# Kernel tuning notes

Hardware: AMD Instinct MI355X
Metric: run time of the kernel (lower is better)

The kernel has to match this reference:

```python
import jax, jax.numpy as jnp
import numpy as np

D_MODEL = 512
NHEAD = 8
HEAD_DIM = D_MODEL // NHEAD
D_FF = 2048
EPS = 1e-5


def _layernorm(x, w, b):
    mu = jnp.mean(x, axis=-1, keepdims=True)
    var = jnp.mean(jnp.square(x - mu), axis=-1, keepdims=True)
    return (x - mu) * jax.lax.rsqrt(var + EPS) * w + b


def setup_inputs() -> dict:
    key = jax.random.key(0)
    ks = jax.random.split(key, 10)
    B, L = 4, 2048
    x = jax.random.normal(ks[0], (B, L, D_MODEL), dtype=jnp.float32)
    attn_bias = jax.random.normal(ks[1], (1, NHEAD, L, L), dtype=jnp.float32)
    s = 0.02
    # weights stored as (in, out): y = x @ w + b
    wq = jax.random.normal(ks[2], (D_MODEL, D_MODEL), dtype=jnp.float32) * s
    wk = jax.random.normal(ks[3], (D_MODEL, D_MODEL), dtype=jnp.float32) * s
    wv = jax.random.normal(ks[4], (D_MODEL, D_MODEL), dtype=jnp.float32) * s
    wo = jax.random.normal(ks[5], (D_MODEL, D_MODEL), dtype=jnp.float32) * s
    w1 = jax.random.normal(ks[6], (D_MODEL, D_FF), dtype=jnp.float32) * s
    w2 = jax.random.normal(ks[7], (D_FF, D_MODEL), dtype=jnp.float32) * s
    z = lambda n: jnp.zeros((n,), dtype=jnp.float32)
    o = lambda n: jnp.ones((n,), dtype=jnp.float32)
    return {
        "x": x, "attn_bias": attn_bias,
        "ln1_w": o(D_MODEL), "ln1_b": z(D_MODEL),
        "ln2_w": o(D_MODEL), "ln2_b": z(D_MODEL),
        "wq": wq, "bq": z(D_MODEL), "wk": wk, "bk": z(D_MODEL),
        "wv": wv, "bv": z(D_MODEL), "wo": wo, "bo": z(D_MODEL),
        "w1": w1, "b1": z(D_FF), "w2": w2, "b2": z(D_MODEL),
    }


def reference(x, attn_bias, ln1_w, ln1_b, ln2_w, ln2_b,
              wq, bq, wk, bk, wv, bv, wo, bo, w1, b1, w2, b2):
    B, L, D = x.shape
    H, Dh = NHEAD, HEAD_DIM

    # --- self-attention block (pre-LN) ---
    h = _layernorm(x, ln1_w, ln1_b)
    q = (h @ wq + bq).reshape(B, L, H, Dh)
    k = (h @ wk + bk).reshape(B, L, H, Dh)
    v = (h @ wv + bv).reshape(B, L, H, Dh)
    scores = jnp.einsum('bqhd,bkhd->bhqk', q, k) * (Dh ** -0.5)
    scores = scores + attn_bias  # broadcast over batch if bias has leading 1
    attn = jax.nn.softmax(scores, axis=-1)
    o = jnp.einsum('bhqk,bkhd->bqhd', attn, v).reshape(B, L, D)
    x = x + (o @ wo + bo)

    # --- feed-forward block (pre-LN, exact GELU like torch nn.GELU) ---
    h2 = _layernorm(x, ln2_w, ln2_b)
    ff = jax.nn.gelu(h2 @ w1 + b1, approximate=False) @ w2 + b2
    return x + ff
```

## Files before the change

### kernel.cpp

```cpp
#include <hip/hip_runtime.h>
#include <hip/hip_bf16.h>

typedef __bf16 bf16x8 __attribute__((ext_vector_type(8)));
typedef float  f32x4  __attribute__((ext_vector_type(4)));
typedef unsigned short us8 __attribute__((ext_vector_type(8)));

__device__ inline unsigned short f2bf(float f) {
    unsigned u = __builtin_bit_cast(unsigned, f);
    u += 0x7fffu + ((u >> 16) & 1u);
    return (unsigned short)(u >> 16);
}

__device__ inline bf16x8 load_frag(const unsigned short* p) {
    return *reinterpret_cast<const bf16x8*>(p);
}

__device__ inline void gload_lds16(const unsigned short* g, unsigned short* l) {
    __builtin_amdgcn_global_load_lds(
        (const __attribute__((address_space(1))) void*)g,
        (__attribute__((address_space(3))) void*)l, 16, 0, 0);
}

__global__ void prep_kernel(const float* __restrict__ wq, const float* __restrict__ wk,
                            const float* __restrict__ wv, const float* __restrict__ wo,
                            const float* __restrict__ w1, const float* __restrict__ w2,
                            const float* __restrict__ bq, const float* __restrict__ bk,
                            const float* __restrict__ bv,
                            unsigned short* __restrict__ wqkvT, unsigned short* __restrict__ woT,
                            unsigned short* __restrict__ w1T, unsigned short* __restrict__ w2T,
                            float* __restrict__ biasqkv) {
    int bid = blockIdx.x;
    int tx = threadIdx.x, ty = threadIdx.y;
    if (bid >= 3072) {
        int i = (bid - 3072) * 256 + ty * 32 + tx;
        float v = (i < 512) ? bq[i] : ((i < 1024) ? bk[i - 512] : bv[i - 1024]);
        biasqkv[i] = v;
        return;
    }
    const float* src; unsigned short* dst; int K, N, tile;
    if (bid < 256)       { src = wq; dst = wqkvT;          K = 512;  N = 512;  tile = bid; }
    else if (bid < 512)  { src = wk; dst = wqkvT + 262144; K = 512;  N = 512;  tile = bid - 256; }
    else if (bid < 768)  { src = wv; dst = wqkvT + 524288; K = 512;  N = 512;  tile = bid - 512; }
    else if (bid < 1024) { src = wo; dst = woT;            K = 512;  N = 512;  tile = bid - 768; }
    else if (bid < 2048) { src = w1; dst = w1T;            K = 512;  N = 2048; tile = bid - 1024; }
    else                 { src = w2; dst = w2T;            K = 2048; N = 512;  tile = bid - 2048; }
    int ntx = N >> 5;
    int n0 = (tile % ntx) * 32, k0 = (tile / ntx) * 32;
    __shared__ float tilebuf[32][33];
#pragma unroll
    for (int i = 0; i < 4; ++i)
        tilebuf[ty + 8 * i][tx] = src[(size_t)(k0 + ty + 8 * i) * N + n0 + tx];
    __syncthreads();
#pragma unroll
    for (int i = 0; i < 4; ++i)
        dst[(size_t)(n0 + ty + 8 * i) * K + k0 + tx] = f2bf(tilebuf[tx][ty + 8 * i]);
}

__global__ __launch_bounds__(256) void ln_kernel(const float* __restrict__ x,
                                                 const float* __restrict__ w,
                                                 const float* __restrict__ b,
                                                 unsigned short* __restrict__ out) {
    int wave = threadIdx.x >> 6, lane = threadIdx.x & 63;
    size_t row = (size_t)blockIdx.x * 4 + wave;
    const float* xp = x + row * 512 + lane * 8;
    float4 v0 = *reinterpret_cast<const float4*>(xp);
    float4 v1 = *reinterpret_cast<const float4*>(xp + 4);
    float s = (v0.x + v0.y) + (v0.z + v0.w) + (v1.x + v1.y) + (v1.z + v1.w);
    float qq = v0.x * v0.x + v0.y * v0.y + v0.z * v0.z + v0.w * v0.w
             + v1.x * v1.x + v1.y * v1.y + v1.z * v1.z + v1.w * v1.w;
#pragma unroll
    for (int off = 1; off < 64; off <<= 1) {
        s += __shfl_xor(s, off, 64);
        qq += __shfl_xor(qq, off, 64);
    }
    float mu = s * (1.0f / 512.0f);
    float var = qq * (1.0f / 512.0f) - mu * mu;
    float rstd = rsqrtf(var + 1e-5f);
    int c = lane * 8;
    float4 w0 = *reinterpret_cast<const float4*>(w + c);
    float4 w1 = *reinterpret_cast<const float4*>(w + c + 4);
    float4 b0 = *reinterpret_cast<const float4*>(b + c);
    float4 b1 = *reinterpret_cast<const float4*>(b + c + 4);
    us8 r;
    r[0] = f2bf((v0.x - mu) * rstd * w0.x + b0.x);
    r[1] = f2bf((v0.y - mu) * rstd * w0.y + b0.y);
    r[2] = f2bf((v0.z - mu) * rstd * w0.z + b0.z);
    r[3] = f2bf((v0.w - mu) * rstd * w0.w + b0.w);
    r[4] = f2bf((v1.x - mu) * rstd * w1.x + b1.x);
    r[5] = f2bf((v1.y - mu) * rstd * w1.y + b1.y);
    r[6] = f2bf((v1.z - mu) * rstd * w1.z + b1.z);
    r[7] = f2bf((v1.w - mu) * rstd * w1.w + b1.w);
    *reinterpret_cast<us8*>(out + row * 512 + c) = r;
}

template <int EPI>
__global__ __launch_bounds__(256) void gemm128(const unsigned short* __restrict__ A,
                                               const unsigned short* __restrict__ BT,
                                               const float* __restrict__ bias, void* Cout,
                                               const float* __restrict__ res, int M, int N, int K) {
    __shared__ unsigned short As[128 * 32];
    __shared__ unsigned short Bs[128 * 32];
    int tid = threadIdx.x;
    int lane = tid & 63, wave = tid >> 6;
    int quad = lane >> 4, l16 = lane & 15;
    int wm = (wave >> 1) * 64, wn = (wave & 1) * 64;
    int m0 = blockIdx.y * 128, n0 = blockIdx.x * 128;

    int c0 = tid, c1 = tid + 256;
    const unsigned short* ag0 = A + (size_t)(m0 + (c0 >> 2)) * K + (c0 & 3) * 8;
    const unsigned short* ag1 = A + (size_t)(m0 + (c1 >> 2)) * K + (c1 & 3) * 8;
    const unsigned short* bg0 = BT + (size_t)(n0 + (c0 >> 2)) * K + (c0 & 3) * 8;
    const unsigned short* bg1 = BT + (size_t)(n0 + (c1 >> 2)) * K + (c1 & 3) * 8;
    unsigned short* al0 = As + c0 * 8;
    unsigned short* al1 = As + c1 * 8;
    unsigned short* bl0 = Bs + c0 * 8;
    unsigned short* bl1 = Bs + c1 * 8;

    f32x4 acc[4][4] = {};
    for (int k0 = 0; k0 < K; k0 += 32) {
        __syncthreads();
        gload_lds16(ag0 + k0, al0);
        gload_lds16(ag1 + k0, al1);
        gload_lds16(bg0 + k0, bl0);
        gload_lds16(bg1 + k0, bl1);
        __syncthreads();
        bf16x8 af[4], bf[4];
#pragma unroll
        for (int i = 0; i < 4; ++i)
            af[i] = load_frag(As + (wm + i * 16 + l16) * 32 + quad * 8);
#pragma unroll
        for (int j = 0; j < 4; ++j)
            bf[j] = load_frag(Bs + (wn + j * 16 + l16) * 32 + quad * 8);
#pragma unroll
        for (int i = 0; i < 4; ++i)
#pragma unroll
            for (int j = 0; j < 4; ++j)
                acc[i][j] = __builtin_amdgcn_mfma_f32_16x16x32_bf16(af[i], bf[j], acc[i][j], 0, 0, 0);
    }

#pragma unroll
    for (int i = 0; i < 4; ++i) {
#pragma unroll
        for (int j = 0; j < 4; ++j) {
#pragma unroll
            for (int r = 0; r < 4; ++r) {
                int m = m0 + wm + i * 16 + quad * 4 + r;
                int n = n0 + wn + j * 16 + l16;
                float val = acc[i][j][r] + bias[n];
                size_t idx = (size_t)m * N + n;
                if (EPI == 0) {
                    ((unsigned short*)Cout)[idx] = f2bf(val);
                } else if (EPI == 1) {
                    ((float*)Cout)[idx] = val + res[idx];
                } else {
                    float g = 0.5f * val * (1.0f + erff(val * 0.70710678118654752f));
                    ((unsigned short*)Cout)[idx] = f2bf(g);
                }
            }
        }
    }
}

__global__ __launch_bounds__(256) void gemm128_ff2(const unsigned short* __restrict__ A,
                                                   const unsigned short* __restrict__ BT,
                                                   const float* __restrict__ bias,
                                                   float* __restrict__ C, int M, int N, int K) {
    __shared__ unsigned short As[128 * 32];
    __shared__ unsigned short Bs[128 * 32];
    int tid = threadIdx.x;
    int lane = tid & 63, wave = tid >> 6;
    int quad = lane >> 4, l16 = lane & 15;
    int wm = (wave >> 1) * 64, wn = (wave & 1) * 64;
    int m0 = blockIdx.y * 128, n0 = blockIdx.x * 128;
    int kbeg = blockIdx.z * (K >> 1), kend = kbeg + (K >> 1);

    int c0 = tid, c1 = tid + 256;
    const unsigned short* ag0 = A + (size_t)(m0 + (c0 >> 2)) * K + (c0 & 3) * 8;
    const unsigned short* ag1 = A + (size_t)(m0 + (c1 >> 2)) * K + (c1 & 3) * 8;
    const unsigned short* bg0 = BT + (size_t)(n0 + (c0 >> 2)) * K + (c0 & 3) * 8;
    const unsigned short* bg1 = BT + (size_t)(n0 + (c1 >> 2)) * K + (c1 & 3) * 8;
    unsigned short* al0 = As + c0 * 8;
    unsigned short* al1 = As + c1 * 8;
    unsigned short* bl0 = Bs + c0 * 8;
    unsigned short* bl1 = Bs + c1 * 8;

    f32x4 acc[4][4] = {};
    for (int k0 = kbeg; k0 < kend; k0 += 32) {
        __syncthreads();
        gload_lds16(ag0 + k0, al0);
        gload_lds16(ag1 + k0, al1);
        gload_lds16(bg0 + k0, bl0);
        gload_lds16(bg1 + k0, bl1);
        __syncthreads();
        bf16x8 af[4], bf[4];
#pragma unroll
        for (int i = 0; i < 4; ++i)
            af[i] = load_frag(As + (wm + i * 16 + l16) * 32 + quad * 8);
#pragma unroll
        for (int j = 0; j < 4; ++j)
            bf[j] = load_frag(Bs + (wn + j * 16 + l16) * 32 + quad * 8);
#pragma unroll
        for (int i = 0; i < 4; ++i)
#pragma unroll
            for (int j = 0; j < 4; ++j)
                acc[i][j] = __builtin_amdgcn_mfma_f32_16x16x32_bf16(af[i], bf[j], acc[i][j], 0, 0, 0);
    }

#pragma unroll
    for (int i = 0; i < 4; ++i) {
#pragma unroll
        for (int j = 0; j < 4; ++j) {
#pragma unroll
            for (int r = 0; r < 4; ++r) {
                int m = m0 + wm + i * 16 + quad * 4 + r;
                int n = n0 + wn + j * 16 + l16;
                float val = acc[i][j][r] + (blockIdx.z == 0 ? bias[n] : 0.0f);
                atomicAdd(&C[(size_t)m * N + n], val);
            }
        }
    }
}

__global__ __launch_bounds__(256) void attn_kernel(const unsigned short* __restrict__ qkv,
                                                   const float* __restrict__ bias,
                                                   unsigned short* __restrict__ o) {
    __shared__ unsigned short Ks[64 * 64];
    __shared__ unsigned short VTs[64 * 72];
    __shared__ unsigned short Ps[4 * 16 * 64];
    const int tid = threadIdx.x;
    const int lane = tid & 63, wave = tid >> 6, quad = lane >> 4, l16 = lane & 15;
    const int qb = blockIdx.x, h = blockIdx.y, b = blockIdx.z;
    const int qw = qb * 64 + wave * 16;

    const unsigned short* qbase = qkv + ((size_t)(b * 2048 + qw + l16)) * 1536 + h * 64 + quad * 8;
    bf16x8 qf0 = load_frag(qbase);
    bf16x8 qf1 = load_frag(qbase + 32);

    f32x4 Oacc[4] = {};
    float lsum[4] = {};

    const int krow0 = wave * 16 + (lane >> 3);
    const int kc_phys = lane & 7;
    unsigned short* kl = Ks + krow0 * 64 + kc_phys * 8;
    const int ksw = (kc_phys ^ (krow0 & 7)) << 3;

    const int srow = tid >> 2, q4 = tid & 3, sd0 = q4 * 16;
    const int vt_c = (srow >> 3) ^ (q4 << 1);
    unsigned short* vtw = VTs + sd0 * 72 + vt_c * 8 + (srow & 7);

    const float* brow = bias + (size_t)h * 2048 * 2048 + (size_t)(qw + quad * 4) * 2048 + l16;

    const float S2 = 0.18033688011112042f;
    const float K2 = 1.4426950408889634f;
    const float C2 = -11.541560327111707f;

    uint4 vt0, vt1;
    float bbf[4][4];
    {
        const unsigned short* kg = qkv + ((size_t)(b * 2048 + krow0)) * 1536 + 512 + h * 64 + ksw;
        gload_lds16(kg, kl);
        gload_lds16(kg + (size_t)8 * 1536, kl + 8 * 64);
        const unsigned short* vg = qkv + ((size_t)(b * 2048 + srow)) * 1536 + 1024 + h * 64 + sd0;
        vt0 = *reinterpret_cast<const uint4*>(vg);
        vt1 = *reinterpret_cast<const uint4*>(vg + 8);
#pragma unroll
        for (int t = 0; t < 4; ++t)
#pragma unroll
            for (int r = 0; r < 4; ++r)
                bbf[t][r] = fmaf(brow[(size_t)r * 2048 + t * 16], K2, C2);
    }

    for (int kt = 0; kt < 32; ++kt) {
        __syncthreads();
        {
            unsigned short vtmp[16];
            *reinterpret_cast<uint4*>(vtmp) = vt0;
            *reinterpret_cast<uint4*>(vtmp + 8) = vt1;
#pragma unroll
            for (int j = 0; j < 16; ++j) vtw[j * 72] = vtmp[j];
        }
        __syncthreads();

#pragma unroll
        for (int t = 0; t < 4; ++t) {
            f32x4 c = {};
            bf16x8 b0 = load_frag(Ks + (t * 16 + l16) * 64 + ((quad ^ (l16 & 7)) << 3));
            bf16x8 b1 = load_frag(Ks + (t * 16 + l16) * 64 + (((quad + 4) ^ (l16 & 7)) << 3));
            c = __builtin_amdgcn_mfma_f32_16x16x32_bf16(qf0, b0, c, 0, 0, 0);
            c = __builtin_amdgcn_mfma_f32_16x16x32_bf16(qf1, b1, c, 0, 0, 0);
            int pc = (t * 2 + (l16 >> 3)) ^ (quad * 2);
            unsigned short* pw = Ps + wave * 1024 + quad * 256 + pc * 8 + (l16 & 7);
#pragma unroll
            for (int r = 0; r < 4; ++r) {
                float e = __builtin_amdgcn_exp2f(fmaf(c[r], S2, bbf[t][r]));
                lsum[r] += e;
                pw[r * 64] = f2bf(e);
            }
        }
        __syncthreads();

        {
            int kb2 = (kt < 31 ? kt + 1 : 31) * 64;
            const unsigned short* kg = qkv + ((size_t)(b * 2048 + kb2 + krow0)) * 1536 + 512 + h * 64 + ksw;
            gload_lds16(kg, kl);
            gload_lds16(kg + (size_t)8 * 1536, kl + 8 * 64);
            const unsigned short* vg = qkv + ((size_t)(b * 2048 + kb2 + srow)) * 1536 + 1024 + h * 64 + sd0;
            vt0 = *reinterpret_cast<const uint4*>(vg);
            vt1 = *reinterpret_cast<const uint4*>(vg + 8);
#pragma unroll
            for (int t = 0; t < 4; ++t)
#pragma unroll
                for (int r = 0; r < 4; ++r)
                    bbf[t][r] = fmaf(brow[(size_t)r * 2048 + kb2 + t * 16], K2, C2);
        }

        bf16x8 pa0 = load_frag(Ps + wave * 1024 + l16 * 64 + ((quad ^ ((l16 >> 2) << 1)) << 3));
        bf16x8 pa1 = load_frag(Ps + wave * 1024 + l16 * 64 + (((quad + 4) ^ ((l16 >> 2) << 1)) << 3));
#pragma unroll
        for (int t = 0; t < 4; ++t) {
            bf16x8 vb0 = load_frag(VTs + (t * 16 + l16) * 72 + ((quad ^ (t * 2)) << 3));
            bf16x8 vb1 = load_frag(VTs + (t * 16 + l16) * 72 + (((quad + 4) ^ (t * 2)) << 3));
            Oacc[t] = __builtin_amdgcn_mfma_f32_16x16x32_bf16(pa0, vb0, Oacc[t], 0, 0, 0);
            Oacc[t] = __builtin_amdgcn_mfma_f32_16x16x32_bf16(pa1, vb1, Oacc[t], 0, 0, 0);
        }
    }

#pragma unroll
    for (int off = 1; off < 16; off <<= 1)
#pragma unroll
        for (int r = 0; r < 4; ++r) lsum[r] += __shfl_xor(lsum[r], off, 64);
#pragma unroll
    for (int r = 0; r < 4; ++r) {
        float inv = 1.0f / lsum[r];
        int qg = qw + quad * 4 + r;
        unsigned short* op = o + ((size_t)(b * 2048 + qg)) * 512 + h * 64;
#pragma unroll
        for (int t = 0; t < 4; ++t) op[t * 16 + l16] = f2bf(Oacc[t][r] * inv);
    }
}

extern "C" void kernel_launch(void* const* d_in, const int* in_sizes, int n_in,
                              void* d_out, int out_size, void* d_ws, size_t ws_size,
                              hipStream_t stream) {
    const float* x      = (const float*)d_in[0];
    const float* abias  = (const float*)d_in[1];
    const float* ln1_w  = (const float*)d_in[2];
    const float* ln1_b  = (const float*)d_in[3];
    const float* ln2_w  = (const float*)d_in[4];
    const float* ln2_b  = (const float*)d_in[5];
    const float* wq     = (const float*)d_in[6];
    const float* bq     = (const float*)d_in[7];
    const float* wk     = (const float*)d_in[8];
    const float* bk     = (const float*)d_in[9];
    const float* wv     = (const float*)d_in[10];
    const float* bv     = (const float*)d_in[11];
    const float* wo     = (const float*)d_in[12];
    const float* bo     = (const float*)d_in[13];
    const float* w1     = (const float*)d_in[14];
    const float* b1     = (const float*)d_in[15];
    const float* w2     = (const float*)d_in[16];
    const float* b2     = (const float*)d_in[17];
    float* out = (float*)d_out;

    char* ws = (char*)d_ws;
    unsigned short* wqkvT  = (unsigned short*)(ws + 0);
    unsigned short* woT    = (unsigned short*)(ws + 1572864);
    unsigned short* w1T    = (unsigned short*)(ws + 2097152);
    unsigned short* w2T    = (unsigned short*)(ws + 4194304);
    float*          biasqkv= (float*)(ws + 6291456);
    unsigned short* hbuf   = (unsigned short*)(ws + 6297600);
    unsigned short* qkv    = (unsigned short*)(ws + 14686208);
    unsigned short* o_attn = (unsigned short*)(ws + 39852032);
    unsigned short* ff1    = (unsigned short*)(ws + 48240640);

    prep_kernel<<<3078, dim3(32, 8), 0, stream>>>(wq, wk, wv, wo, w1, w2, bq, bk, bv,
                                                  wqkvT, woT, w1T, w2T, biasqkv);
    ln_kernel<<<2048, 256, 0, stream>>>(x, ln1_w, ln1_b, hbuf);
    gemm128<0><<<dim3(12, 64), 256, 0, stream>>>(hbuf, wqkvT, biasqkv, qkv, nullptr, 8192, 1536, 512);
    attn_kernel<<<dim3(32, 8, 4), 256, 0, stream>>>(qkv, abias, o_attn);
    gemm128<1><<<dim3(4, 64), 256, 0, stream>>>(o_attn, woT, bo, out, x, 8192, 512, 512);
    ln_kernel<<<2048, 256, 0, stream>>>(out, ln2_w, ln2_b, hbuf);
    gemm128<2><<<dim3(16, 64), 256, 0, stream>>>(hbuf, w1T, b1, ff1, nullptr, 8192, 2048, 512);
    gemm128_ff2<<<dim3(4, 64, 2), 256, 0, stream>>>(ff1, w2T, b2, out, 8192, 512, 2048);
}
```

Baseline: 494.9 us.

## Rework GEMMs with 64-wide swizzled K tiles, V-transposed layout, double-buffered attention

The GEMM core now stages 64-wide K tiles with an XOR-swizzled LDS layout. Each GEMM gets its own specialised epilogue kernel, and occupancy hints are added through launch bounds. The QKV projection writes V pre-transposed to a separate buffer, so attention can load K and V^T straight into double-buffered LDS with async loads instead of transposing V through registers each tile. The output projection becomes a split-K atomic GEMM that adds into an output first seeded with x by a device copy. This adds an extra memcpy and atomics in exchange for fewer barriers and less LDS traffic.

```diff
diff --git a/kernel.cpp b/kernel.cpp
--- a/kernel.cpp
+++ b/kernel.cpp
@@ -93,233 +93,237 @@
     *reinterpret_cast<us8*>(out + row * 512 + c) = r;
 }
 
-template <int EPI>
-__global__ __launch_bounds__(256) void gemm128(const unsigned short* __restrict__ A,
-                                               const unsigned short* __restrict__ BT,
-                                               const float* __restrict__ bias, void* Cout,
-                                               const float* __restrict__ res, int M, int N, int K) {
-    __shared__ unsigned short As[128 * 32];
-    __shared__ unsigned short Bs[128 * 32];
-    int tid = threadIdx.x;
-    int lane = tid & 63, wave = tid >> 6;
-    int quad = lane >> 4, l16 = lane & 15;
-    int wm = (wave >> 1) * 64, wn = (wave & 1) * 64;
-    int m0 = blockIdx.y * 128, n0 = blockIdx.x * 128;
-
-    int c0 = tid, c1 = tid + 256;
-    const unsigned short* ag0 = A + (size_t)(m0 + (c0 >> 2)) * K + (c0 & 3) * 8;
-    const unsigned short* ag1 = A + (size_t)(m0 + (c1 >> 2)) * K + (c1 & 3) * 8;
-    const unsigned short* bg0 = BT + (size_t)(n0 + (c0 >> 2)) * K + (c0 & 3) * 8;
-    const unsigned short* bg1 = BT + (size_t)(n0 + (c1 >> 2)) * K + (c1 & 3) * 8;
-    unsigned short* al0 = As + c0 * 8;
-    unsigned short* al1 = As + c1 * 8;
-    unsigned short* bl0 = Bs + c0 * 8;
-    unsigned short* bl1 = Bs + c1 * 8;
-
+__device__ __forceinline__ void gemm_core(const unsigned short* __restrict__ A,
+                                          const unsigned short* __restrict__ BT,
+                                          int K, int kbeg, int ksteps,
+                                          int m0, int n0, f32x4 (&acc)[4][4]) {
+    __shared__ unsigned short As[8192];
+    __shared__ unsigned short Bs[8192];
+    const int tid = threadIdx.x;
+    const int lane = tid & 63, wave = tid >> 6;
+    const int quad = lane >> 4, l16 = lane & 15;
+    const int wm = (wave >> 1) * 64, wn = (wave & 1) * 64;
+    const int row0 = tid >> 3;
+    const int jl = (tid & 7) ^ (row0 & 7);
+    const unsigned short* ag = A + (size_t)(m0 + row0) * K + kbeg + jl * 8;
+    const unsigned short* bg = BT + (size_t)(n0 + row0) * K + kbeg + jl * 8;
+    unsigned short* al = As + tid * 8;
+    unsigned short* bl = Bs + tid * 8;
+    const int sw = l16 & 7;
+
+    for (int ks = 0; ks < ksteps; ++ks) {
+        __syncthreads();
+#pragma unroll
+        for (int s = 0; s < 4; ++s) {
+            gload_lds16(ag + (size_t)32 * s * K, al + 2048 * s);
+            gload_lds16(bg + (size_t)32 * s * K, bl + 2048 * s);
+        }
+        ag += 64; bg += 64;
+        __syncthreads();
+#pragma unroll
+        for (int h = 0; h < 2; ++h) {
+            bf16x8 af[4], bf[4];
+#pragma unroll
+            for (int i = 0; i < 4; ++i)
+                af[i] = load_frag(As + (wm + i * 16 + l16) * 64 + (((h * 4 + quad) ^ sw) * 8));
+#pragma unroll
+            for (int j = 0; j < 4; ++j)
+                bf[j] = load_frag(Bs + (wn + j * 16 + l16) * 64 + (((h * 4 + quad) ^ sw) * 8));
+#pragma unroll
+            for (int i = 0; i < 4; ++i)
+#pragma unroll
+                for (int j = 0; j < 4; ++j)
+                    acc[i][j] = __builtin_amdgcn_mfma_f32_16x16x32_bf16(af[i], bf[j], acc[i][j], 0, 0, 0);
+        }
+    }
+}
+
+__global__ __launch_bounds__(256, 3) void gemm_qkv_k(const unsigned short* __restrict__ A,
+                                                     const unsigned short* __restrict__ BT,
+                                                     const float* __restrict__ bias,
+                                                     unsigned short* __restrict__ qk,
+                                                     unsigned short* __restrict__ vT) {
     f32x4 acc[4][4] = {};
-    for (int k0 = 0; k0 < K; k0 += 32) {
-        __syncthreads();
-        gload_lds16(ag0 + k0, al0);
-        gload_lds16(ag1 + k0, al1);
-        gload_lds16(bg0 + k0, bl0);
-        gload_lds16(bg1 + k0, bl1);
-        __syncthreads();
-        bf16x8 af[4], bf[4];
+    const int m0 = blockIdx.y * 128, n0 = blockIdx.x * 128;
+    gemm_core(A, BT, 512, 0, 8, m0, n0, acc);
+    const int tid = threadIdx.x, lane = tid & 63, wave = tid >> 6;
+    const int quad = lane >> 4, l16 = lane & 15;
+    const int wm = (wave >> 1) * 64, wn = (wave & 1) * 64;
+    if (n0 < 1024) {
 #pragma unroll
         for (int i = 0; i < 4; ++i)
-            af[i] = load_frag(As + (wm + i * 16 + l16) * 32 + quad * 8);
-#pragma unroll
-        for (int j = 0; j < 4; ++j)
-            bf[j] = load_frag(Bs + (wn + j * 16 + l16) * 32 + quad * 8);
-#pragma unroll
-        for (int i = 0; i < 4; ++i)
-#pragma unroll
-            for (int j = 0; j < 4; ++j)
-                acc[i][j] = __builtin_amdgcn_mfma_f32_16x16x32_bf16(af[i], bf[j], acc[i][j], 0, 0, 0);
-    }
-
-#pragma unroll
-    for (int i = 0; i < 4; ++i) {
+#pragma unroll
+            for (int j = 0; j < 4; ++j) {
+                int n = n0 + wn + j * 16 + l16;
+                float bn = bias[n];
+#pragma unroll
+                for (int r = 0; r < 4; ++r) {
+                    int m = m0 + wm + i * 16 + quad * 4 + r;
+                    qk[(size_t)m * 1024 + n] = f2bf(acc[i][j][r] + bn);
+                }
+            }
+    } else {
+#pragma unroll
+        for (int i = 0; i < 4; ++i) {
+            int mb = m0 + wm + i * 16 + quad * 4;
+            int bb = mb >> 11, tok = mb & 2047;
+#pragma unroll
+            for (int j = 0; j < 4; ++j) {
+                int n = n0 + wn + j * 16 + l16;
+                float bn = bias[n];
+                int hd = n - 1024;
+                ushort4 pk;
+                pk.x = f2bf(acc[i][j][0] + bn);
+                pk.y = f2bf(acc[i][j][1] + bn);
+                pk.z = f2bf(acc[i][j][2] + bn);
+                pk.w = f2bf(acc[i][j][3] + bn);
+                *reinterpret_cast<ushort4*>(vT + (size_t)(bb * 512 + hd) * 2048 + tok) = pk;
+            }
+        }
+    }
+}
+
+__global__ __launch_bounds__(256, 3) void gemm_gelu_k(const unsigned short* __restrict__ A,
+                                                      const unsigned short* __restrict__ BT,
+                                                      const float* __restrict__ bias,
+                                                      unsigned short* __restrict__ C) {
+    f32x4 acc[4][4] = {};
+    const int m0 = blockIdx.y * 128, n0 = blockIdx.x * 128;
+    gemm_core(A, BT, 512, 0, 8, m0, n0, acc);
+    const int tid = threadIdx.x, lane = tid & 63, wave = tid >> 6;
+    const int quad = lane >> 4, l16 = lane & 15;
+    const int wm = (wave >> 1) * 64, wn = (wave & 1) * 64;
+#pragma unroll
+    for (int i = 0; i < 4; ++i)
 #pragma unroll
         for (int j = 0; j < 4; ++j) {
+            int n = n0 + wn + j * 16 + l16;
+            float bn = bias[n];
 #pragma unroll
             for (int r = 0; r < 4; ++r) {
                 int m = m0 + wm + i * 16 + quad * 4 + r;
-                int n = n0 + wn + j * 16 + l16;
-                float val = acc[i][j][r] + bias[n];
-                size_t idx = (size_t)m * N + n;
-                if (EPI == 0) {
-                    ((unsigned short*)Cout)[idx] = f2bf(val);
-                } else if (EPI == 1) {
-                    ((float*)Cout)[idx] = val + res[idx];
-                } else {
-                    float g = 0.5f * val * (1.0f + erff(val * 0.70710678118654752f));
-                    ((unsigned short*)Cout)[idx] = f2bf(g);
-                }
-            }
-        }
-    }
-}
-
-__global__ __launch_bounds__(256) void gemm128_ff2(const unsigned short* __restrict__ A,
-                                                   const unsigned short* __restrict__ BT,
-                                                   const float* __restrict__ bias,
-                                                   float* __restrict__ C, int M, int N, int K) {
-    __shared__ unsigned short As[128 * 32];
-    __shared__ unsigned short Bs[128 * 32];
-    int tid = threadIdx.x;
-    int lane = tid & 63, wave = tid >> 6;
-    int quad = lane >> 4, l16 = lane & 15;
-    int wm = (wave >> 1) * 64, wn = (wave & 1) * 64;
-    int m0 = blockIdx.y * 128, n0 = blockIdx.x * 128;
-    int kbeg = blockIdx.z * (K >> 1), kend = kbeg + (K >> 1);
-
-    int c0 = tid, c1 = tid + 256;
-    const unsigned short* ag0 = A + (size_t)(m0 + (c0 >> 2)) * K + (c0 & 3) * 8;
-    const unsigned short* ag1 = A + (size_t)(m0 + (c1 >> 2)) * K + (c1 & 3) * 8;
-    const unsigned short* bg0 = BT + (size_t)(n0 + (c0 >> 2)) * K + (c0 & 3) * 8;
-    const unsigned short* bg1 = BT + (size_t)(n0 + (c1 >> 2)) * K + (c1 & 3) * 8;
-    unsigned short* al0 = As + c0 * 8;
-    unsigned short* al1 = As + c1 * 8;
-    unsigned short* bl0 = Bs + c0 * 8;
-    unsigned short* bl1 = Bs + c1 * 8;
-
+                float val = acc[i][j][r] + bn;
+                float g = 0.5f * val * (1.0f + erff(val * 0.70710678118654752f));
+                C[(size_t)m * 2048 + n] = f2bf(g);
+            }
+        }
+}
+
+__global__ __launch_bounds__(256, 3) void gemm_atomic_k(const unsigned short* __restrict__ A,
+                                                        const unsigned short* __restrict__ BT,
+                                                        const float* __restrict__ bias,
+                                                        float* __restrict__ C,
+                                                        int N, int K, int ksteps) {
     f32x4 acc[4][4] = {};
-    for (int k0 = kbeg; k0 < kend; k0 += 32) {
-        __syncthreads();
-        gload_lds16(ag0 + k0, al0);
-        gload_lds16(ag1 + k0, al1);
-        gload_lds16(bg0 + k0, bl0);
-        gload_lds16(bg1 + k0, bl1);
-        __syncthreads();
-        bf16x8 af[4], bf[4];
-#pragma unroll
-        for (int i = 0; i < 4; ++i)
-            af[i] = load_frag(As + (wm + i * 16 + l16) * 32 + quad * 8);
-#pragma unroll
-        for (int j = 0; j < 4; ++j)
-            bf[j] = load_frag(Bs + (wn + j * 16 + l16) * 32 + quad * 8);
-#pragma unroll
-        for (int i = 0; i < 4; ++i)
-#pragma unroll
-            for (int j = 0; j < 4; ++j)
-                acc[i][j] = __builtin_amdgcn_mfma_f32_16x16x32_bf16(af[i], bf[j], acc[i][j], 0, 0, 0);
-    }
-
-#pragma unroll
-    for (int i = 0; i < 4; ++i) {
+    const int m0 = blockIdx.y * 128, n0 = blockIdx.x * 128;
+    const int kbeg = blockIdx.z * ksteps * 64;
+    gemm_core(A, BT, K, kbeg, ksteps, m0, n0, acc);
+    const int tid = threadIdx.x, lane = tid & 63, wave = tid >> 6;
+    const int quad = lane >> 4, l16 = lane & 15;
+    const int wm = (wave >> 1) * 64, wn = (wave & 1) * 64;
+    const bool addb = (blockIdx.z == 0);
+#pragma unroll
+    for (int i = 0; i < 4; ++i)
 #pragma unroll
         for (int j = 0; j < 4; ++j) {
+            int n = n0 + wn + j * 16 + l16;
+            float bn = addb ? bias[n] : 0.0f;
 #pragma unroll
             for (int r = 0; r < 4; ++r) {
                 int m = m0 + wm + i * 16 + quad * 4 + r;
-                int n = n0 + wn + j * 16 + l16;
-                float val = acc[i][j][r] + (blockIdx.z == 0 ? bias[n] : 0.0f);
-                atomicAdd(&C[(size_t)m * N + n], val);
-            }
-        }
-    }
-}
-
-__global__ __launch_bounds__(256) void attn_kernel(const unsigned short* __restrict__ qkv,
-                                                   const float* __restrict__ bias,
-                                                   unsigned short* __restrict__ o) {
-    __shared__ unsigned short Ks[64 * 64];
-    __shared__ unsigned short VTs[64 * 72];
-    __shared__ unsigned short Ps[4 * 16 * 64];
+                atomicAdd(&C[(size_t)m * N + n], acc[i][j][r] + bn);
+            }
+        }
+}
+
+__global__ __launch_bounds__(256, 4) void attn_kernel(const unsigned short* __restrict__ qk,
+                                                      const unsigned short* __restrict__ vT,
+                                                      const float* __restrict__ bias,
+                                                      unsigned short* __restrict__ o) {
+    __shared__ unsigned short Ks[2][4096];
+    __shared__ unsigned short VTs[2][4096];
+    __shared__ unsigned short Ps[4096];
     const int tid = threadIdx.x;
     const int lane = tid & 63, wave = tid >> 6, quad = lane >> 4, l16 = lane & 15;
     const int qb = blockIdx.x, h = blockIdx.y, b = blockIdx.z;
     const int qw = qb * 64 + wave * 16;
 
-    const unsigned short* qbase = qkv + ((size_t)(b * 2048 + qw + l16)) * 1536 + h * 64 + quad * 8;
+    const unsigned short* qbase = qk + (size_t)(b * 2048 + qw + l16) * 1024 + h * 64 + quad * 8;
     bf16x8 qf0 = load_frag(qbase);
     bf16x8 qf1 = load_frag(qbase + 32);
 
     f32x4 Oacc[4] = {};
     float lsum[4] = {};
 
-    const int krow0 = wave * 16 + (lane >> 3);
-    const int kc_phys = lane & 7;
-    unsigned short* kl = Ks + krow0 * 64 + kc_phys * 8;
-    const int ksw = (kc_phys ^ (krow0 & 7)) << 3;
-
-    const int srow = tid >> 2, q4 = tid & 3, sd0 = q4 * 16;
-    const int vt_c = (srow >> 3) ^ (q4 << 1);
-    unsigned short* vtw = VTs + sd0 * 72 + vt_c * 8 + (srow & 7);
+    const int p8 = lane & 7;
+    const int r0 = wave * 16 + (lane >> 3);
+    const int swz = (p8 ^ (r0 & 7)) * 8;
+    const unsigned short* kg = qk + (size_t)(b * 2048 + r0) * 1024 + 512 + h * 64 + swz;
+    const unsigned short* vg = vT + (size_t)(b * 512 + h * 64 + r0) * 2048 + swz;
+    const int ldst = r0 * 64 + p8 * 8;
 
     const float* brow = bias + (size_t)h * 2048 * 2048 + (size_t)(qw + quad * 4) * 2048 + l16;
-
     const float S2 = 0.18033688011112042f;
     const float K2 = 1.4426950408889634f;
     const float C2 = -11.541560327111707f;
 
-    uint4 vt0, vt1;
+    gload_lds16(kg, Ks[0] + ldst);
+    gload_lds16(kg + 8 * 1024, Ks[0] + 512 + ldst);
+    gload_lds16(vg, VTs[0] + ldst);
+    gload_lds16(vg + 8 * 2048, VTs[0] + 512 + ldst);
     float bbf[4][4];
-    {
-        const unsigned short* kg = qkv + ((size_t)(b * 2048 + krow0)) * 1536 + 512 + h * 64 + ksw;
-        gload_lds16(kg, kl);
-        gload_lds16(kg + (size_t)8 * 1536, kl + 8 * 64);
-        const unsigned short* vg = qkv + ((size_t)(b * 2048 + srow)) * 1536 + 1024 + h * 64 + sd0;
-        vt0 = *reinterpret_cast<const uint4*>(vg);
-        vt1 = *reinterpret_cast<const uint4*>(vg + 8);
-#pragma unroll
-        for (int t = 0; t < 4; ++t)
-#pragma unroll
-            for (int r = 0; r < 4; ++r)
-                bbf[t][r] = fmaf(brow[(size_t)r * 2048 + t * 16], K2, C2);
-    }
-
+#pragma unroll
+    for (int t = 0; t < 4; ++t)
+#pragma unroll
+        for (int r = 0; r < 4; ++r)
+            bbf[t][r] = fmaf(brow[(size_t)r * 2048 + t * 16], K2, C2);
+
+    const int sw7 = l16 & 7;
     for (int kt = 0; kt < 32; ++kt) {
+        const int buf = kt & 1;
         __syncthreads();
-        {
-            unsigned short vtmp[16];
-            *reinterpret_cast<uint4*>(vtmp) = vt0;
-            *reinterpret_cast<uint4*>(vtmp + 8) = vt1;
-#pragma unroll
-            for (int j = 0; j < 16; ++j) vtw[j * 72] = vtmp[j];
-        }
-        __syncthreads();
-
+        if (kt < 31) {
+            const unsigned short* kg2 = kg + (size_t)(kt + 1) * 64 * 1024;
+            const unsigned short* vg2 = vg + (kt + 1) * 64;
+            gload_lds16(kg2, Ks[buf ^ 1] + ldst);
+            gload_lds16(kg2 + 8 * 1024, Ks[buf ^ 1] + 512 + ldst);
+            gload_lds16(vg2, VTs[buf ^ 1] + ldst);
+            gload_lds16(vg2 + 8 * 2048, VTs[buf ^ 1] + 512 + ldst);
+        }
 #pragma unroll
         for (int t = 0; t < 4; ++t) {
+            const unsigned short* krow = Ks[buf] + (t * 16 + l16) * 64;
+            bf16x8 kb0 = load_frag(krow + ((quad ^ sw7) * 8));
+            bf16x8 kb1 = load_frag(krow + (((quad + 4) ^ sw7) * 8));
             f32x4 c = {};
-            bf16x8 b0 = load_frag(Ks + (t * 16 + l16) * 64 + ((quad ^ (l16 & 7)) << 3));
-            bf16x8 b1 = load_frag(Ks + (t * 16 + l16) * 64 + (((quad + 4) ^ (l16 & 7)) << 3));
-            c = __builtin_amdgcn_mfma_f32_16x16x32_bf16(qf0, b0, c, 0, 0, 0);
-            c = __builtin_amdgcn_mfma_f32_16x16x32_bf16(qf1, b1, c, 0, 0, 0);
-            int pc = (t * 2 + (l16 >> 3)) ^ (quad * 2);
-            unsigned short* pw = Ps + wave * 1024 + quad * 256 + pc * 8 + (l16 & 7);
+            c = __builtin_amdgcn_mfma_f32_16x16x32_bf16(qf0, kb0, c, 0, 0, 0);
+            c = __builtin_amdgcn_mfma_f32_16x16x32_bf16(qf1, kb1, c, 0, 0, 0);
 #pragma unroll
             for (int r = 0; r < 4; ++r) {
                 float e = __builtin_amdgcn_exp2f(fmaf(c[r], S2, bbf[t][r]));
                 lsum[r] += e;
-                pw[r * 64] = f2bf(e);
+                int m = quad * 4 + r;
+                int phys = (t * 2 + (l16 >> 3)) ^ ((m >> 1) & 7);
+                Ps[wave * 1024 + m * 64 + phys * 8 + (l16 & 7)] = f2bf(e);
             }
         }
         __syncthreads();
-
-        {
-            int kb2 = (kt < 31 ? kt + 1 : 31) * 64;
-            const unsigned short* kg = qkv + ((size_t)(b * 2048 + kb2 + krow0)) * 1536 + 512 + h * 64 + ksw;
-            gload_lds16(kg, kl);
-            gload_lds16(kg + (size_t)8 * 1536, kl + 8 * 64);
-            const unsigned short* vg = qkv + ((size_t)(b * 2048 + kb2 + srow)) * 1536 + 1024 + h * 64 + sd0;
-            vt0 = *reinterpret_cast<const uint4*>(vg);
-            vt1 = *reinterpret_cast<const uint4*>(vg + 8);
+        if (kt < 31) {
+            const float* b2 = brow + (size_t)(kt + 1) * 64;
 #pragma unroll
             for (int t = 0; t < 4; ++t)
 #pragma unroll
                 for (int r = 0; r < 4; ++r)
-                    bbf[t][r] = fmaf(brow[(size_t)r * 2048 + kb2 + t * 16], K2, C2);
-        }
-
-        bf16x8 pa0 = load_frag(Ps + wave * 1024 + l16 * 64 + ((quad ^ ((l16 >> 2) << 1)) << 3));
-        bf16x8 pa1 = load_frag(Ps + wave * 1024 + l16 * 64 + (((quad + 4) ^ ((l16 >> 2) << 1)) << 3));
+                    bbf[t][r] = fmaf(b2[(size_t)r * 2048 + t * 16], K2, C2);
+        }
+        const unsigned short* prow = Ps + wave * 1024 + l16 * 64;
+        bf16x8 pa0 = load_frag(prow + ((quad ^ ((l16 >> 1) & 7)) * 8));
+        bf16x8 pa1 = load_frag(prow + (((quad + 4) ^ ((l16 >> 1) & 7)) * 8));
 #pragma unroll
         for (int t = 0; t < 4; ++t) {
-            bf16x8 vb0 = load_frag(VTs + (t * 16 + l16) * 72 + ((quad ^ (t * 2)) << 3));
-            bf16x8 vb1 = load_frag(VTs + (t * 16 + l16) * 72 + (((quad + 4) ^ (t * 2)) << 3));
+            const unsigned short* vrow = VTs[buf] + (t * 16 + l16) * 64;
+            bf16x8 vb0 = load_frag(vrow + ((quad ^ sw7) * 8));
+            bf16x8 vb1 = load_frag(vrow + (((quad + 4) ^ sw7) * 8));
             Oacc[t] = __builtin_amdgcn_mfma_f32_16x16x32_bf16(pa0, vb0, Oacc[t], 0, 0, 0);
             Oacc[t] = __builtin_amdgcn_mfma_f32_16x16x32_bf16(pa1, vb1, Oacc[t], 0, 0, 0);
         }
@@ -333,7 +337,7 @@
     for (int r = 0; r < 4; ++r) {
         float inv = 1.0f / lsum[r];
         int qg = qw + quad * 4 + r;
-        unsigned short* op = o + ((size_t)(b * 2048 + qg)) * 512 + h * 64;
+        unsigned short* op = o + (size_t)(b * 2048 + qg) * 512 + h * 64;
 #pragma unroll
         for (int t = 0; t < 4; ++t) op[t * 16 + l16] = f2bf(Oacc[t][r] * inv);
     }
@@ -369,17 +373,19 @@
     unsigned short* w2T    = (unsigned short*)(ws + 4194304);
     float*          biasqkv= (float*)(ws + 6291456);
     unsigned short* hbuf   = (unsigned short*)(ws + 6297600);
-    unsigned short* qkv    = (unsigned short*)(ws + 14686208);
+    unsigned short* qkbuf  = (unsigned short*)(ws + 14686208);
+    unsigned short* vTbuf  = (unsigned short*)(ws + 31463424);
     unsigned short* o_attn = (unsigned short*)(ws + 39852032);
     unsigned short* ff1    = (unsigned short*)(ws + 48240640);
 
+    hipMemcpyAsync(out, x, (size_t)8192 * 512 * sizeof(float), hipMemcpyDeviceToDevice, stream);
     prep_kernel<<<3078, dim3(32, 8), 0, stream>>>(wq, wk, wv, wo, w1, w2, bq, bk, bv,
                                                   wqkvT, woT, w1T, w2T, biasqkv);
     ln_kernel<<<2048, 256, 0, stream>>>(x, ln1_w, ln1_b, hbuf);
-    gemm128<0><<<dim3(12, 64), 256, 0, stream>>>(hbuf, wqkvT, biasqkv, qkv, nullptr, 8192, 1536, 512);
-    attn_kernel<<<dim3(32, 8, 4), 256, 0, stream>>>(qkv, abias, o_attn);
-    gemm128<1><<<dim3(4, 64), 256, 0, stream>>>(o_attn, woT, bo, out, x, 8192, 512, 512);
+    gemm_qkv_k<<<dim3(12, 64), 256, 0, stream>>>(hbuf, wqkvT, biasqkv, qkbuf, vTbuf);
+    attn_kernel<<<dim3(32, 8, 4), 256, 0, stream>>>(qkbuf, vTbuf, abias, o_attn);
+    gemm_atomic_k<<<dim3(4, 64, 2), 256, 0, stream>>>(o_attn, woT, bo, out, 512, 512, 4);
     ln_kernel<<<2048, 256, 0, stream>>>(out, ln2_w, ln2_b, hbuf);
-    gemm128<2><<<dim3(16, 64), 256, 0, stream>>>(hbuf, w1T, b1, ff1, nullptr, 8192, 2048, 512);
-    gemm128_ff2<<<dim3(4, 64, 2), 256, 0, stream>>>(ff1, w2T, b2, out, 8192, 512, 2048);
-}
+    gemm_gelu_k<<<dim3(16, 64), 256, 0, stream>>>(hbuf, w1T, b1, ff1);
+    gemm_atomic_k<<<dim3(4, 64, 2), 256, 0, stream>>>(ff1, w2T, b2, out, 512, 2048, 16);
+}
```

After: 426.7 us. -13.8%, faster.
